# Kernel tuning notes

Measured on AMD Instinct MI355X. Metric: run time of the kernel, lower is better.

The kernel has to match this reference:

```python
import jax, jax.numpy as jnp
import numpy as np

B, S, D = 4, 2048, 1024
NEG_BIG = -1.0e9


def setup_inputs() -> dict:
    key = jax.random.key(0)
    ks = jax.random.split(key, 9)
    scale = 1.0 / np.sqrt(D)
    inp = {
        "v": jax.random.normal(ks[0], (B, S, D), dtype=jnp.float32),
        "k": jax.random.normal(ks[1], (B, S, D), dtype=jnp.float32),
        "q": jax.random.normal(ks[2], (B, S, D), dtype=jnp.float32),
        # causal mask: 1 where attention is disallowed (j > i), broadcast over batch
        "mask": jnp.triu(jnp.ones((1, S, S), dtype=jnp.float32), k=1),
        "Wq": jax.random.normal(ks[3], (D, D), dtype=jnp.float32) * scale,
        "bq": jnp.zeros((D,), dtype=jnp.float32),
        "Wk": jax.random.normal(ks[4], (D, D), dtype=jnp.float32) * scale,
        "bk": jnp.zeros((D,), dtype=jnp.float32),
        "Wv": jax.random.normal(ks[5], (D, D), dtype=jnp.float32) * scale,
        "bv": jnp.zeros((D,), dtype=jnp.float32),
    }
    return inp


def reference(v, k, q, mask, Wq, bq, Wk, bk, Wv, bv):
    # Dense projections (Keras Dense: x @ W + b)
    qp = q @ Wq + bq  # [B, S, D]
    kp = k @ Wk + bk  # [B, S, D]
    vp = v @ Wv + bv  # [B, S, D]

    dk = jnp.asarray(D, dtype=qp.dtype)
    logits = jnp.einsum("bqd,bkd->bqk", qp, kp) / jnp.sqrt(dk)  # [B, S, S]
    logits = logits + mask * NEG_BIG
    attn = jax.nn.softmax(logits, axis=-1)  # [B, S, S]
    out = jnp.einsum("bqk,bkd->bqd", attn, vp)  # [B, S, D]
    return out, attn
```

## Files before the change

### kernel.cpp

```cpp
#include <hip/hip_runtime.h>
#include <hip/hip_bf16.h>
#include <cstdint>

#define BATCH 4
#define S_LEN 2048
#define D_DIM 1024

typedef __attribute__((ext_vector_type(4))) float f32x4_t;
typedef __attribute__((ext_vector_type(8))) __bf16 bf16x8_t;

__device__ __forceinline__ ushort f32_to_bf16(float f) {
    uint32_t u = __float_as_uint(f);
    uint32_t r = (u + 0x7FFFu + ((u >> 16) & 1u)) >> 16;
    return (ushort)r;
}

__global__ __launch_bounds__(256)
void cvt_all_kernel(const float* __restrict__ q, const float* __restrict__ k,
                    const float* __restrict__ v, const float* __restrict__ wk,
                    const float* __restrict__ wq,
                    ushort* __restrict__ xqkv, ushort* __restrict__ xw, int n4) {
    int z = blockIdx.y;
    const float* src;
    ushort* dst;
    int n;
    if (z < 3) {
        src = (z == 0) ? q : ((z == 1) ? k : v);
        dst = xqkv + (size_t)z * n4 * 4;
        n = n4;
    } else {
        src = nullptr; dst = nullptr; n = 0;
    }
    int idx = blockIdx.x * blockDim.x + threadIdx.x;
    int stride = gridDim.x * blockDim.x;
    if (z < 3) {
        const float4* in4 = (const float4*)src;
        ushort4* out4 = (ushort4*)dst;
        for (int i = idx; i < n; i += stride) {
            float4 vv = in4[i];
            ushort4 o;
            o.x = f32_to_bf16(vv.x);
            o.y = f32_to_bf16(vv.y);
            o.z = f32_to_bf16(vv.z);
            o.w = f32_to_bf16(vv.w);
            out4[i] = o;
        }
    } else {
        int nw = D_DIM * D_DIM / 4;
        const float4* ik = (const float4*)wk;
        const float4* iq = (const float4*)wq;
        ushort4* ok = (ushort4*)xw;
        ushort4* oq = (ushort4*)(xw + (size_t)D_DIM * D_DIM);
        for (int i = idx; i < nw; i += stride) {
            float4 a = ik[i];
            ushort4 o;
            o.x = f32_to_bf16(a.x); o.y = f32_to_bf16(a.y);
            o.z = f32_to_bf16(a.z); o.w = f32_to_bf16(a.w);
            ok[i] = o;
            float4 b = iq[i];
            o.x = f32_to_bf16(b.x); o.y = f32_to_bf16(b.y);
            o.z = f32_to_bf16(b.z); o.w = f32_to_bf16(b.w);
            oq[i] = o;
        }
    }
}

__global__ __launch_bounds__(256)
void transpose_cvt_kernel(const float* __restrict__ in, ushort* __restrict__ out,
                          int rows, int cols) {
    __shared__ ushort tile[64][66];
    int r0 = blockIdx.y * 64, c0 = blockIdx.x * 64;
    int t = threadIdx.x;
    int cr = t & 63;
    int cc = t >> 6;
    #pragma unroll
    for (int i = 0; i < 16; ++i) {
        int r = cc * 16 + i;
        tile[r][cr] = f32_to_bf16(in[(size_t)(r0 + r) * cols + (c0 + cr)]);
    }
    __syncthreads();
    #pragma unroll
    for (int i = 0; i < 16; ++i) {
        int c = cc * 16 + i;
        out[(size_t)(c0 + c) * rows + (r0 + cr)] = tile[cr][c];
    }
}

__global__ __launch_bounds__(256)
void fill_kernel(const float* __restrict__ bv, float* __restrict__ bias2) {
    int i = blockIdx.x * blockDim.x + threadIdx.x;
    bias2[i] = (i < D_DIM) ? 0.f : bv[i - D_DIM];
}

__global__ __launch_bounds__(256)
void hv_kernel(const float* __restrict__ Wk, const float* __restrict__ bq,
               float* __restrict__ hv) {
    int wave = threadIdx.x >> 6, lane = threadIdx.x & 63;
    int r = blockIdx.x * 4 + wave;
    const float* row = Wk + (size_t)r * D_DIM;
    float s = 0.f;
    #pragma unroll
    for (int it = 0; it < 16; ++it)
        s += row[it * 64 + lane] * bq[it * 64 + lane];
    #pragma unroll
    for (int off = 32; off > 0; off >>= 1)
        s += __shfl_xor(s, off);
    if (lane == 0) hv[r] = s;
}

__global__ __launch_bounds__(256)
void wvec_kernel(const ushort* __restrict__ xk, const float* __restrict__ hv,
                 float* __restrict__ w) {
    int wave = threadIdx.x >> 6, lane = threadIdx.x & 63;
    int r = blockIdx.x * 4 + wave;
    const ushort* row = xk + (size_t)r * D_DIM + lane * 16;
    const float* hp = hv + lane * 16;
    float s = 0.f;
    #pragma unroll
    for (int it = 0; it < 16; ++it) {
        uint32_t u = row[it];
        s += __uint_as_float(u << 16) * hp[it];
    }
    #pragma unroll
    for (int off = 32; off > 0; off >>= 1)
        s += __shfl_xor(s, off);
    if (lane == 0) w[r] = s * 0.03125f;
}

enum { MODE_PROJ = 0, MODE_MT = 1, MODE_LOGITS = 2 };

#define PRE_BAR() do { __builtin_amdgcn_s_barrier(); \
    asm volatile("s_waitcnt lgkmcnt(0)" ::: "memory"); \
    __builtin_amdgcn_sched_barrier(0); } while (0)
#define POST_BAR() do { __builtin_amdgcn_sched_barrier(0); \
    __builtin_amdgcn_s_barrier(); } while (0)
#define GATE(N) do { asm volatile("s_waitcnt vmcnt(" #N ")" ::: "memory"); \
    __builtin_amdgcn_sched_barrier(0); } while (0)

#define GLOAD(dst, src) __builtin_amdgcn_global_load_lds( \
    (const __attribute__((address_space(1))) uint32_t*)(src), \
    (__attribute__((address_space(3))) uint32_t*)(dst), 16, 0, 0)

__device__ __forceinline__ void xcd_swizzle(int& bc, int& br) {
    int gx = gridDim.x;
    int nwg = gx * gridDim.y;
    int orig = blockIdx.y * gx + blockIdx.x;
    int xcd = orig & 7, idx = orig >> 3;
    int wgid = xcd * (nwg >> 3) + idx;
    bc = wgid % gx;
    br = wgid / gx;
}

template<int MODE>
__global__ __launch_bounds__(512, 2)
void gemm_q_kernel(const ushort* __restrict__ A, const ushort* __restrict__ Bt,
                   const float* __restrict__ bias, void* __restrict__ Cout,
                   ushort* __restrict__ vpTp,
                   int K, int lda, int ldb, int ldc,
                   long strideA, long strideC, float scale) {
    __shared__ ushort As[2][256 * 64];
    __shared__ ushort Bs[2][256 * 64];
    int bc, br;
    xcd_swizzle(bc, br);
    int bz = blockIdx.z;
    if (MODE == MODE_LOGITS && bc > br) return;
    const ushort* Ab = (MODE == MODE_PROJ) ? A + (size_t)(bc >> 2) * strideA
                                           : A + (size_t)bz * strideA;
    const ushort* Bb = (MODE == MODE_LOGITS) ? Bt + (size_t)bz * strideA : Bt;
    int brow = br * 256, bcol = bc * 256;
    int t = threadIdx.x, lane = t & 63, wid = t >> 6;
    int wr = wid >> 2, wc = wid & 3;
    int nkt = K / 64;

    const ushort* aSrc[4];
    const ushort* bSrc[4];
    int oL[4];
    #pragma unroll
    for (int j = 0; j < 4; ++j) {
        int o = (j * 512 + t) * 16;
        int row = o >> 7;
        int colb = (o & 127) ^ ((row & 7) << 4);
        oL[j] = o >> 1;
        aSrc[j] = Ab + (size_t)(brow + row) * lda + (colb >> 1);
        bSrc[j] = Bb + (size_t)(bcol + row) * ldb + (colb >> 1);
    }
    auto stgA = [&](int tk, int slot, int j0, int j1) {
        ushort* d = &As[slot][0];
        GLOAD(d + oL[j0], aSrc[j0] + tk * 64);
        GLOAD(d + oL[j1], aSrc[j1] + tk * 64);
    };
    auto stgB = [&](int tk, int slot, int j0, int j1) {
        ushort* d = &Bs[slot][0];
        GLOAD(d + oL[j0], bSrc[j0] + tk * 64);
        GLOAD(d + oL[j1], bSrc[j1] + tk * 64);
    };

    int rdA[2][4], rdB[4];
    #pragma unroll
    for (int mh = 0; mh < 2; ++mh)
        #pragma unroll
        for (int m = 0; m < 4; ++m) {
            int ra = wr * 128 + mh * 64 + m * 16 + (lane & 15);
            int cb = (lane >> 4) * 16;
            rdA[mh][m] = ra * 128 + (cb ^ ((ra & 7) << 4));
        }
    #pragma unroll
    for (int nf = 0; nf < 4; ++nf) {
        int rb = (nf >> 1) * 128 + wc * 32 + (nf & 1) * 16 + (lane & 15);
        int cb = (lane >> 4) * 16;
        rdB[nf] = rb * 128 + (cb ^ ((rb & 7) << 4));
    }

    f32x4_t acc[8][4];
    #pragma unroll
    for (int m = 0; m < 8; ++m)
        #pragma unroll
        for (int n = 0; n < 4; ++n)
            acc[m][n] = (f32x4_t){0.f, 0.f, 0.f, 0.f};

    bf16x8_t af[4][2], bfr[4][2];

    auto readAh = [&](int slot, int mh) {
        const char* base = (const char*)&As[slot][0];
        #pragma unroll
        for (int m = 0; m < 4; ++m) {
            af[m][0] = *(const bf16x8_t*)(base + rdA[mh][m]);
            af[m][1] = *(const bf16x8_t*)(base + (rdA[mh][m] ^ 64));
        }
    };
    auto readBh = [&](int slot, int nh) {
        const char* base = (const char*)&Bs[slot][0];
        #pragma unroll
        for (int n = 0; n < 2; ++n) {
            int nf = nh * 2 + n;
            bfr[nf][0] = *(const bf16x8_t*)(base + rdB[nf]);
            bfr[nf][1] = *(const bf16x8_t*)(base + (rdB[nf] ^ 64));
        }
    };

#define QUAD(MH, NH)                                                                \
    do { __builtin_amdgcn_s_setprio(1);                                             \
        _Pragma("unroll") for (int m = 0; m < 4; ++m)                               \
        _Pragma("unroll") for (int n = 0; n < 2; ++n)                               \
        _Pragma("unroll") for (int ks = 0; ks < 2; ++ks)                            \
            acc[(MH) * 4 + m][(NH) * 2 + n] = __builtin_amdgcn_mfma_f32_16x16x32_bf16( \
                af[m][ks], bfr[(NH) * 2 + n][ks], acc[(MH) * 4 + m][(NH) * 2 + n], 0, 0, 0); \
        __builtin_amdgcn_s_setprio(0); } while (0)

    stgB(0, 0, 0, 1); stgA(0, 0, 0, 2); stgB(0, 0, 2, 3); stgA(0, 0, 1, 3);
    GATE(4);
    __builtin_amdgcn_s_barrier();

    for (int y = 0; y < nkt; ++y) {
        int cur = y & 1, nxt = cur ^ 1;
        bool st = (y + 1 < nkt);
        readAh(cur, 0); readBh(cur, 0);
        if (st) stgB(y + 1, nxt, 0, 1);
        PRE_BAR(); QUAD(0, 0);
        if (st) { GATE(4); } else { GATE(2); }
        POST_BAR();
        readBh(cur, 1);
        if (st) stgA(y + 1, nxt, 0, 2);
        PRE_BAR(); QUAD(0, 1);
        if (st) { GATE(4); } else { GATE(0); }
        POST_BAR();
        readAh(cur, 1);
        if (st) stgB(y + 1, nxt, 2, 3);
        PRE_BAR(); QUAD(1, 1); POST_BAR();
        if (st) stgA(y + 1, nxt, 1, 3);
        PRE_BAR(); QUAD(1, 0);
        if (st) { GATE(4); }
        POST_BAR();
    }
#undef QUAD

    int crow0 = brow + wr * 128 + ((lane >> 4) * 4);
    int ccol0 = wc * 32 + (lane & 15);
    if (MODE == MODE_PROJ) {
        #pragma unroll
        for (int mf = 0; mf < 8; ++mf) {
            int rowg = crow0 + (mf >> 2) * 64 + (mf & 3) * 16;
            #pragma unroll
            for (int nf = 0; nf < 4; ++nf) {
                int gcol = bcol + (nf >> 1) * 128 + ccol0 + (nf & 1) * 16;
                float bv = bias[gcol];
                if (gcol < D_DIM) {
                    ushort* C = (ushort*)Cout;
                    #pragma unroll
                    for (int j = 0; j < 4; ++j)
                        C[(size_t)(rowg + j) * D_DIM + gcol] = f32_to_bf16(acc[mf][nf][j] + bv);
                } else {
                    int d = gcol - D_DIM;
                    int b = rowg >> 11, s = rowg & 2047;
                    ushort4 o;
                    o.x = f32_to_bf16(acc[mf][nf][0] + bv);
                    o.y = f32_to_bf16(acc[mf][nf][1] + bv);
                    o.z = f32_to_bf16(acc[mf][nf][2] + bv);
                    o.w = f32_to_bf16(acc[mf][nf][3] + bv);
                    *(ushort4*)&vpTp[((size_t)b * D_DIM + d) * S_LEN + s] = o;
                }
            }
        }
    } else if (MODE == MODE_MT) {
        ushort* C = (ushort*)Cout;
        #pragma unroll
        for (int mf = 0; mf < 8; ++mf) {
            int rowg = crow0 + (mf >> 2) * 64 + (mf & 3) * 16;
            #pragma unroll
            for (int nf = 0; nf < 4; ++nf) {
                int gcol = bcol + (nf >> 1) * 128 + ccol0 + (nf & 1) * 16;
                #pragma unroll
                for (int j = 0; j < 4; ++j)
                    C[(size_t)(rowg + j) * ldc + gcol] = f32_to_bf16(acc[mf][nf][j]);
            }
        }
    } else {
        float* C = (float*)Cout + (size_t)bz * strideC;
        #pragma unroll
        for (int mf = 0; mf < 8; ++mf) {
            int rowg = crow0 + (mf >> 2) * 64 + (mf & 3) * 16;
            #pragma unroll
            for (int nf = 0; nf < 4; ++nf) {
                int col = bcol + (nf >> 1) * 128 + ccol0 + (nf & 1) * 16;
                #pragma unroll
                for (int j = 0; j < 4; ++j)
                    C[(size_t)(rowg + j) * ldc + col] = acc[mf][nf][j] * scale;
            }
        }
    }
}

#define LGKM(N) do { asm volatile("s_waitcnt lgkmcnt(" #N ")" ::: "memory"); \
    __builtin_amdgcn_sched_barrier(0); } while (0)

__global__ __launch_bounds__(512, 2)
void gemm_out_kernel(const ushort* __restrict__ A, const ushort* __restrict__ Bt,
                     void* __restrict__ Cout,
                     int K, int lda, int ldb, int ldc,
                     long strideA, long strideB, long strideC, float scale) {
    __shared__ ushort As[3][256 * 64];
    __shared__ ushort Bs[3][128 * 64];
    int bc, br;
    xcd_swizzle(bc, br);
    int bz = blockIdx.z;
    const ushort* Ab = A + (size_t)bz * strideA;
    const ushort* Bb = Bt + (size_t)bz * strideB;
    int brow = br * 256, bcol = bc * 128;
    int t = threadIdx.x, lane = t & 63, wid = t >> 6;
    int wr = wid >> 1, wc = wid & 1;
    int nkt = min(K / 64, (brow + 256) / 64);

    const ushort* aSrc[4];
    const ushort* bSrc[2];
    int oA[4], oB[2];
    #pragma unroll
    for (int j = 0; j < 4; ++j) {
        int o = (j * 512 + t) * 16;
        int row = o >> 7;
        int col = (o & 127) ^ ((row & 7) << 4);
        oA[j] = o >> 1;
        aSrc[j] = Ab + (size_t)(brow + row) * lda + (col >> 1);
    }
    #pragma unroll
    for (int j = 0; j < 2; ++j) {
        int o = (j * 512 + t) * 16;
        int row = o >> 7;
        int col = (o & 127) ^ ((row & 7) << 4);
        oB[j] = o >> 1;
        bSrc[j] = Bb + (size_t)(bcol + row) * ldb + (col >> 1);
    }
    auto stage = [&](int tk, int slot) {
        ushort* dA = &As[slot][0];
        ushort* dB = &Bs[slot][0];
        #pragma unroll
        for (int j = 0; j < 4; ++j) GLOAD(dA + oA[j], aSrc[j] + tk * 64);
        #pragma unroll
        for (int j = 0; j < 2; ++j) GLOAD(dB + oB[j], bSrc[j] + tk * 64);
    };

    int rdA[4][2], rdB[4][2];
    #pragma unroll
    for (int m = 0; m < 4; ++m) {
        int ra = wr * 64 + m * 16 + (lane & 15);
        #pragma unroll
        for (int ks = 0; ks < 2; ++ks) {
            int cb = ks * 64 + ((lane >> 4) * 16);
            rdA[m][ks] = ra * 128 + (cb ^ ((ra & 7) << 4));
        }
    }
    #pragma unroll
    for (int n = 0; n < 4; ++n) {
        int rb = wc * 64 + n * 16 + (lane & 15);
        #pragma unroll
        for (int ks = 0; ks < 2; ++ks) {
            int cb = ks * 64 + ((lane >> 4) * 16);
            rdB[n][ks] = rb * 128 + (cb ^ ((rb & 7) << 4));
        }
    }

    f32x4_t acc[4][4];
    #pragma unroll
    for (int m = 0; m < 4; ++m)
        #pragma unroll
        for (int n = 0; n < 4; ++n)
            acc[m][n] = (f32x4_t){0.f, 0.f, 0.f, 0.f};

    bf16x8_t aE0[4], aE1[4], bE0[4], bE1[4];
    bf16x8_t aO0[4], aO1[4], bO0[4], bO1[4];

#define MF16(AV, BV)                                                           \
    do { __builtin_amdgcn_s_setprio(1);                                        \
        _Pragma("unroll") for (int m = 0; m < 4; ++m)                          \
        _Pragma("unroll") for (int n = 0; n < 4; ++n)                          \
            acc[m][n] = __builtin_amdgcn_mfma_f32_16x16x32_bf16(               \
                AV[m], BV[n], acc[m][n], 0, 0, 0);                             \
        __builtin_amdgcn_s_setprio(0); } while (0)

#define TILE_BODY(X, CA0, CA1, CB0, CB1, NA0, NA1, NB0, NB1)                   \
    do {                                                                       \
        int x_ = (X);                                                          \
        __builtin_amdgcn_s_barrier();                                          \
        if (x_ + 2 < nkt) stage(x_ + 2, (x_ + 2) % 3);                         \
        if (x_ + 1 < nkt) { if (x_ + 2 < nkt) { GATE(6); } else { GATE(0); } } \
        __builtin_amdgcn_s_barrier();                                          \
        {                                                                      \
            const char* nA = (const char*)&As[(x_ + 1) % 3][0];                \
            const char* nB = (const char*)&Bs[(x_ + 1) % 3][0];                \
            if (x_ + 1 < nkt) {                                                \
                _Pragma("unroll") for (int n = 0; n < 4; ++n)                  \
                    NB0[n] = *(const bf16x8_t*)(nB + rdB[n][0]);               \
                _Pragma("unroll") for (int m = 0; m < 4; ++m)                  \
                    NA0[m] = *(const bf16x8_t*)(nA + rdA[m][0]);               \
                LGKM(8);                                                       \
            } else { LGKM(0); }                                                \
            MF16(CA0, CB0);                                                    \
            if (x_ + 1 < nkt) {                                                \
                _Pragma("unroll") for (int n = 0; n < 4; ++n)                  \
                    NB1[n] = *(const bf16x8_t*)(nB + rdB[n][1]);               \
                _Pragma("unroll") for (int m = 0; m < 4; ++m)                  \
                    NA1[m] = *(const bf16x8_t*)(nA + rdA[m][1]);               \
            }                                                                  \
            MF16(CA1, CB1);                                                    \
        }                                                                      \
    } while (0)

    stage(0, 0);
    stage(1, 1);
    GATE(6);
    __builtin_amdgcn_s_barrier();
    {
        const char* pA = (const char*)&As[0][0];
        const char* pB = (const char*)&Bs[0][0];
        #pragma unroll
        for (int n = 0; n < 4; ++n) bE0[n] = *(const bf16x8_t*)(pB + rdB[n][0]);
        #pragma unroll
        for (int m = 0; m < 4; ++m) aE0[m] = *(const bf16x8_t*)(pA + rdA[m][0]);
        #pragma unroll
        for (int n = 0; n < 4; ++n) bE1[n] = *(const bf16x8_t*)(pB + rdB[n][1]);
        #pragma unroll
        for (int m = 0; m < 4; ++m) aE1[m] = *(const bf16x8_t*)(pA + rdA[m][1]);
    }

    int nhalf = nkt >> 1;
    for (int it = 0; it < nhalf; ++it) {
        int x = 2 * it;
        TILE_BODY(x,     aE0, aE1, bE0, bE1, aO0, aO1, bO0, bO1);
        TILE_BODY(x + 1, aO0, aO1, bO0, bO1, aE0, aE1, bE0, bE1);
    }
#undef TILE_BODY
#undef MF16

    float* C = (float*)Cout + (size_t)bz * strideC;
    int crow0 = brow + wr * 64 + ((lane >> 4) * 4);
    int ccol0 = bcol + wc * 64 + (lane & 15);
    #pragma unroll
    for (int mf = 0; mf < 4; ++mf)
        #pragma unroll
        for (int nf = 0; nf < 4; ++nf) {
            int col = ccol0 + nf * 16;
            #pragma unroll
            for (int j = 0; j < 4; ++j) {
                int rowg = crow0 + mf * 16 + j;
                C[(size_t)rowg * ldc + col] = acc[mf][nf][j] * scale;
            }
        }
}

__global__ __launch_bounds__(256)
void softmax_causal_kernel(float* __restrict__ attn, ushort* __restrict__ attn_bf,
                           const float* __restrict__ w) {
    int rowid = blockIdx.x;
    int i = rowid & (S_LEN - 1);
    float* lrow = attn + (size_t)rowid * S_LEN;
    ushort* brw = attn_bf + (size_t)rowid * S_LEN;
    const float* wv = w + (rowid & ~(S_LEN - 1));
    int t = threadIdx.x;
    int nvalid = i + 1;
    int nact = (nvalid + 255) >> 8;

    float vals[8];
    float lmax = -1e30f;
    #pragma unroll
    for (int it = 0; it < 8; ++it) {
        if (it < nact) {
            int j = it * 256 + t;
            float v = (j < nvalid) ? (lrow[j] + wv[j]) : -1e30f;
            vals[it] = v;
            lmax = fmaxf(lmax, v);
        }
    }
    #pragma unroll
    for (int off = 32; off > 0; off >>= 1)
        lmax = fmaxf(lmax, __shfl_xor(lmax, off));

    __shared__ float redm[4];
    __shared__ float reds[4];
    int wave = t >> 6, lane = t & 63;
    if (lane == 0) redm[wave] = lmax;
    __syncthreads();
    float m = fmaxf(fmaxf(redm[0], redm[1]), fmaxf(redm[2], redm[3]));

    float lsum = 0.f;
    #pragma unroll
    for (int it = 0; it < 8; ++it) {
        if (it < nact) {
            int j = it * 256 + t;
            float e = (j < nvalid) ? __expf(vals[it] - m) : 0.f;
            vals[it] = e;
            lsum += e;
        }
    }
    #pragma unroll
    for (int off = 32; off > 0; off >>= 1)
        lsum += __shfl_xor(lsum, off);
    if (lane == 0) reds[wave] = lsum;
    __syncthreads();
    float denom = reds[0] + reds[1] + reds[2] + reds[3];
    float inv = 1.f / denom;

    #pragma unroll
    for (int it = 0; it < 8; ++it) {
        int j = it * 256 + t;
        if (it < nact) {
            float p = vals[it] * inv;
            lrow[j] = p;
            brw[j] = f32_to_bf16(p);
        } else {
            lrow[j] = 0.f;
        }
    }
}

extern "C" void kernel_launch(void* const* d_in, const int* in_sizes, int n_in,
                              void* d_out, int out_size, void* d_ws, size_t ws_size,
                              hipStream_t stream) {
    const float* v  = (const float*)d_in[0];
    const float* k  = (const float*)d_in[1];
    const float* q  = (const float*)d_in[2];
    const float* Wq = (const float*)d_in[4];
    const float* bq = (const float*)d_in[5];
    const float* Wk = (const float*)d_in[6];
    const float* Wv = (const float*)d_in[8];
    const float* bv = (const float*)d_in[9];

    float* out  = (float*)d_out;
    float* attn = (float*)d_out + (size_t)BATCH * S_LEN * D_DIM;

    char* ws = (char*)d_ws;
    const size_t MB = 1024u * 1024u;
    const size_t NTOK = (size_t)BATCH * S_LEN;
    ushort* xqkv  = (ushort*)(ws);
    ushort* xq    = xqkv;
    ushort* xk    = xqkv + NTOK * D_DIM;
    ushort* qq    = (ushort*)(ws + 48 * MB);
    ushort* vpT   = (ushort*)(ws + 64 * MB);
    ushort* Bcat  = (ushort*)(ws + 80 * MB);
    ushort* xW    = (ushort*)(ws + 84 * MB);
    float*  bias2 = (float*)(ws + 88 * MB);
    float*  hvb   = (float*)(ws + 88 * MB + 8192);
    float*  wvec  = (float*)(ws + 88 * MB + 16384);
    ushort* attn_bf = (ushort*)(ws);

    const int n4 = (int)(NTOK * D_DIM / 4);
    cvt_all_kernel<<<dim3(1024, 4), dim3(256), 0, stream>>>(q, k, v, Wk, Wq, xqkv, xW, n4);
    transpose_cvt_kernel<<<dim3(16, 16), dim3(256), 0, stream>>>(Wv, Bcat + (size_t)D_DIM * D_DIM, D_DIM, D_DIM);
    fill_kernel<<<dim3(8), dim3(256), 0, stream>>>(bv, bias2);
    hv_kernel<<<dim3(256), dim3(256), 0, stream>>>(Wk, bq, hvb);
    wvec_kernel<<<dim3(2048), dim3(256), 0, stream>>>(xk, hvb, wvec);

    gemm_q_kernel<MODE_MT><<<dim3(4, 4, 1), dim3(512), 0, stream>>>(
        xW, xW + (size_t)D_DIM * D_DIM, nullptr, Bcat, nullptr,
        D_DIM, D_DIM, D_DIM, D_DIM, 0, 0, 1.f);

    gemm_q_kernel<MODE_PROJ><<<dim3(8, 32, 1), dim3(512), 0, stream>>>(
        xqkv, Bcat, bias2, qq, vpT,
        D_DIM, D_DIM, D_DIM, 2048, (long)2 * NTOK * D_DIM, 0, 1.f);

    gemm_q_kernel<MODE_LOGITS><<<dim3(8, 8, BATCH), dim3(512), 0, stream>>>(
        qq, xk, nullptr, attn, nullptr,
        D_DIM, D_DIM, D_DIM, S_LEN,
        (long)S_LEN * D_DIM, (long)S_LEN * S_LEN, 0.03125f);

    softmax_causal_kernel<<<dim3((int)NTOK), dim3(256), 0, stream>>>(attn, attn_bf, wvec);

    gemm_out_kernel<<<dim3(8, 8, BATCH), dim3(512), 0, stream>>>(
        attn_bf, vpT, out, S_LEN, S_LEN, S_LEN, D_DIM,
        (long)S_LEN * S_LEN, (long)D_DIM * S_LEN, (long)S_LEN * D_DIM, 1.f);
}
```

Before: 219.6 us.

## Split-K the weight-product and causal logits GEMMs to fill more CUs

```diff
diff --git a/kernel.cpp b/kernel.cpp
--- a/kernel.cpp
+++ b/kernel.cpp
@@ -1,5 +1,6 @@
 #include <hip/hip_runtime.h>
 #include <hip/hip_bf16.h>
+#include <hip/hip_fp16.h>
 #include <cstdint>
 
 #define BATCH 4
@@ -13,6 +14,14 @@
     uint32_t u = __float_as_uint(f);
     uint32_t r = (u + 0x7FFFu + ((u >> 16) & 1u)) >> 16;
     return (ushort)r;
+}
+__device__ __forceinline__ ushort f32_to_f16(float f) {
+    __half h = __float2half(f);
+    return *(ushort*)&h;
+}
+__device__ __forceinline__ float f16_to_f32(ushort u) {
+    __half h = *(__half*)&u;
+    return __half2float(h);
 }
 
 __global__ __launch_bounds__(256)
@@ -21,22 +30,14 @@
                     const float* __restrict__ wq,
                     ushort* __restrict__ xqkv, ushort* __restrict__ xw, int n4) {
     int z = blockIdx.y;
-    const float* src;
-    ushort* dst;
-    int n;
-    if (z < 3) {
-        src = (z == 0) ? q : ((z == 1) ? k : v);
-        dst = xqkv + (size_t)z * n4 * 4;
-        n = n4;
-    } else {
-        src = nullptr; dst = nullptr; n = 0;
-    }
     int idx = blockIdx.x * blockDim.x + threadIdx.x;
     int stride = gridDim.x * blockDim.x;
     if (z < 3) {
+        const float* src = (z == 0) ? q : ((z == 1) ? k : v);
+        ushort* dst = xqkv + (size_t)z * n4 * 4;
         const float4* in4 = (const float4*)src;
         ushort4* out4 = (ushort4*)dst;
-        for (int i = idx; i < n; i += stride) {
+        for (int i = idx; i < n4; i += stride) {
             float4 vv = in4[i];
             ushort4 o;
             o.x = f32_to_bf16(vv.x);
@@ -127,6 +128,22 @@
     if (lane == 0) w[r] = s * 0.03125f;
 }
 
+__global__ __launch_bounds__(256)
+void mt_reduce_kernel(const ushort* __restrict__ p, ushort* __restrict__ M) {
+    int i = blockIdx.x * 1024 + threadIdx.x * 4;
+    const size_t N = (size_t)D_DIM * D_DIM;
+    ushort4 a = *(const ushort4*)&p[i];
+    ushort4 b = *(const ushort4*)&p[N + i];
+    ushort4 c = *(const ushort4*)&p[2 * N + i];
+    ushort4 d = *(const ushort4*)&p[3 * N + i];
+    ushort4 o;
+    o.x = f32_to_bf16(f16_to_f32(a.x) + f16_to_f32(b.x) + f16_to_f32(c.x) + f16_to_f32(d.x));
+    o.y = f32_to_bf16(f16_to_f32(a.y) + f16_to_f32(b.y) + f16_to_f32(c.y) + f16_to_f32(d.y));
+    o.z = f32_to_bf16(f16_to_f32(a.z) + f16_to_f32(b.z) + f16_to_f32(c.z) + f16_to_f32(d.z));
+    o.w = f32_to_bf16(f16_to_f32(a.w) + f16_to_f32(b.w) + f16_to_f32(c.w) + f16_to_f32(d.w));
+    *(ushort4*)&M[i] = o;
+}
+
 enum { MODE_PROJ = 0, MODE_MT = 1, MODE_LOGITS = 2 };
 
 #define PRE_BAR() do { __builtin_amdgcn_s_barrier(); \
@@ -155,15 +172,37 @@
 __global__ __launch_bounds__(512, 2)
 void gemm_q_kernel(const ushort* __restrict__ A, const ushort* __restrict__ Bt,
                    const float* __restrict__ bias, void* __restrict__ Cout,
-                   ushort* __restrict__ vpTp,
+                   ushort* __restrict__ aux,
                    int K, int lda, int ldb, int ldc,
                    long strideA, long strideC, float scale) {
     __shared__ ushort As[2][256 * 64];
     __shared__ ushort Bs[2][256 * 64];
-    int bc, br;
-    xcd_swizzle(bc, br);
-    int bz = blockIdx.z;
-    if (MODE == MODE_LOGITS && bc > br) return;
+
+    int bc, br, bz = 0, kh = 0, tri = 0, koff = 0;
+    if (MODE == MODE_PROJ) {
+        xcd_swizzle(bc, br);
+    } else {
+        int nwg = gridDim.x;
+        int orig = blockIdx.x;
+        int widx = (orig & 7) * (nwg >> 3) + (orig >> 3);
+        if (MODE == MODE_MT) {
+            kh = widx & 3;
+            int tile = widx >> 2;
+            bc = tile & 3;
+            br = tile >> 2;
+            koff = kh << 8;
+        } else {
+            kh = widx & 1;
+            int rest = widx >> 1;
+            bz = rest / 36;
+            tri = rest - bz * 36;
+            br = 0;
+            while ((br + 1) * (br + 2) / 2 <= tri) ++br;
+            bc = tri - br * (br + 1) / 2;
+            koff = kh << 9;
+        }
+    }
+
     const ushort* Ab = (MODE == MODE_PROJ) ? A + (size_t)(bc >> 2) * strideA
                                            : A + (size_t)bz * strideA;
     const ushort* Bb = (MODE == MODE_LOGITS) ? Bt + (size_t)bz * strideA : Bt;
@@ -181,8 +220,8 @@
         int row = o >> 7;
         int colb = (o & 127) ^ ((row & 7) << 4);
         oL[j] = o >> 1;
-        aSrc[j] = Ab + (size_t)(brow + row) * lda + (colb >> 1);
-        bSrc[j] = Bb + (size_t)(bcol + row) * ldb + (colb >> 1);
+        aSrc[j] = Ab + (size_t)(brow + row) * lda + (colb >> 1) + koff;
+        bSrc[j] = Bb + (size_t)(bcol + row) * ldb + (colb >> 1) + koff;
     }
     auto stgA = [&](int tk, int slot, int j0, int j1) {
         ushort* d = &As[slot][0];
@@ -274,15 +313,15 @@
     }
 #undef QUAD
 
-    int crow0 = brow + wr * 128 + ((lane >> 4) * 4);
-    int ccol0 = wc * 32 + (lane & 15);
+    int lrow0 = wr * 128 + ((lane >> 4) * 4);
+    int lcol0 = wc * 32 + (lane & 15);
     if (MODE == MODE_PROJ) {
         #pragma unroll
         for (int mf = 0; mf < 8; ++mf) {
-            int rowg = crow0 + (mf >> 2) * 64 + (mf & 3) * 16;
+            int rowg = brow + lrow0 + (mf >> 2) * 64 + (mf & 3) * 16;
             #pragma unroll
             for (int nf = 0; nf < 4; ++nf) {
-                int gcol = bcol + (nf >> 1) * 128 + ccol0 + (nf & 1) * 16;
+                int gcol = bcol + (nf >> 1) * 128 + lcol0 + (nf & 1) * 16;
                 float bv = bias[gcol];
                 if (gcol < D_DIM) {
                     ushort* C = (ushort*)Cout;
@@ -297,34 +336,49 @@
                     o.y = f32_to_bf16(acc[mf][nf][1] + bv);
                     o.z = f32_to_bf16(acc[mf][nf][2] + bv);
                     o.w = f32_to_bf16(acc[mf][nf][3] + bv);
-                    *(ushort4*)&vpTp[((size_t)b * D_DIM + d) * S_LEN + s] = o;
+                    *(ushort4*)&aux[((size_t)b * D_DIM + d) * S_LEN + s] = o;
                 }
             }
         }
     } else if (MODE == MODE_MT) {
-        ushort* C = (ushort*)Cout;
+        ushort* P = aux + (size_t)kh * D_DIM * D_DIM;
         #pragma unroll
         for (int mf = 0; mf < 8; ++mf) {
-            int rowg = crow0 + (mf >> 2) * 64 + (mf & 3) * 16;
+            int rowg = brow + lrow0 + (mf >> 2) * 64 + (mf & 3) * 16;
             #pragma unroll
             for (int nf = 0; nf < 4; ++nf) {
-                int gcol = bcol + (nf >> 1) * 128 + ccol0 + (nf & 1) * 16;
+                int gcol = bcol + (nf >> 1) * 128 + lcol0 + (nf & 1) * 16;
                 #pragma unroll
                 for (int j = 0; j < 4; ++j)
-                    C[(size_t)(rowg + j) * ldc + gcol] = f32_to_bf16(acc[mf][nf][j]);
+                    P[(size_t)(rowg + j) * D_DIM + gcol] = f32_to_f16(acc[mf][nf][j]);
             }
         }
     } else {
-        float* C = (float*)Cout + (size_t)bz * strideC;
-        #pragma unroll
-        for (int mf = 0; mf < 8; ++mf) {
-            int rowg = crow0 + (mf >> 2) * 64 + (mf & 3) * 16;
+        if (kh == 0) {
+            float* C = (float*)Cout + (size_t)bz * strideC;
             #pragma unroll
-            for (int nf = 0; nf < 4; ++nf) {
-                int col = bcol + (nf >> 1) * 128 + ccol0 + (nf & 1) * 16;
+            for (int mf = 0; mf < 8; ++mf) {
+                int rowg = brow + lrow0 + (mf >> 2) * 64 + (mf & 3) * 16;
                 #pragma unroll
-                for (int j = 0; j < 4; ++j)
-                    C[(size_t)(rowg + j) * ldc + col] = acc[mf][nf][j] * scale;
+                for (int nf = 0; nf < 4; ++nf) {
+                    int col = bcol + (nf >> 1) * 128 + lcol0 + (nf & 1) * 16;
+                    #pragma unroll
+                    for (int j = 0; j < 4; ++j)
+                        C[(size_t)(rowg + j) * ldc + col] = acc[mf][nf][j] * scale;
+                }
+            }
+        } else {
+            ushort* P = aux + ((size_t)(bz * 36 + tri) << 16);
+            #pragma unroll
+            for (int mf = 0; mf < 8; ++mf) {
+                int lr = lrow0 + (mf >> 2) * 64 + (mf & 3) * 16;
+                #pragma unroll
+                for (int nf = 0; nf < 4; ++nf) {
+                    int lc = (nf >> 1) * 128 + lcol0 + (nf & 1) * 16;
+                    #pragma unroll
+                    for (int j = 0; j < 4; ++j)
+                        P[(size_t)(lr + j) * 256 + lc] = f32_to_f16(acc[mf][nf][j] * scale);
+                }
             }
         }
     }
@@ -488,15 +542,17 @@
 
 __global__ __launch_bounds__(256)
 void softmax_causal_kernel(float* __restrict__ attn, ushort* __restrict__ attn_bf,
-                           const float* __restrict__ w) {
+                           const float* __restrict__ w, const ushort* __restrict__ lgp) {
     int rowid = blockIdx.x;
+    int bz = rowid >> 11;
     int i = rowid & (S_LEN - 1);
+    int br = i >> 8;
     float* lrow = attn + (size_t)rowid * S_LEN;
     ushort* brw = attn_bf + (size_t)rowid * S_LEN;
     const float* wv = w + (rowid & ~(S_LEN - 1));
     int t = threadIdx.x;
     int nvalid = i + 1;
-    int nact = (nvalid + 255) >> 8;
+    int nact = br + 1;
 
     float vals[8];
     float lmax = -1e30f;
@@ -504,7 +560,9 @@
     for (int it = 0; it < 8; ++it) {
         if (it < nact) {
             int j = it * 256 + t;
-            float v = (j < nvalid) ? (lrow[j] + wv[j]) : -1e30f;
+            int tri = br * (br + 1) / 2 + it;
+            float lp = f16_to_f32(lgp[((size_t)(bz * 36 + tri) << 16) + ((i & 255) << 8) + t]);
+            float v = (j < nvalid) ? (lrow[j] + lp + wv[j]) : -1e30f;
             vals[it] = v;
             lmax = fmaxf(lmax, v);
         }
@@ -570,15 +628,16 @@
     const size_t MB = 1024u * 1024u;
     const size_t NTOK = (size_t)BATCH * S_LEN;
     ushort* xqkv  = (ushort*)(ws);
-    ushort* xq    = xqkv;
     ushort* xk    = xqkv + NTOK * D_DIM;
     ushort* qq    = (ushort*)(ws + 48 * MB);
     ushort* vpT   = (ushort*)(ws + 64 * MB);
     ushort* Bcat  = (ushort*)(ws + 80 * MB);
     ushort* xW    = (ushort*)(ws + 84 * MB);
-    float*  bias2 = (float*)(ws + 88 * MB);
-    float*  hvb   = (float*)(ws + 88 * MB + 8192);
-    float*  wvec  = (float*)(ws + 88 * MB + 16384);
+    ushort* mtp   = (ushort*)(ws + 88 * MB);
+    ushort* lgp   = (ushort*)(ws + 80 * MB);
+    float*  bias2 = (float*)(ws + 99 * MB);
+    float*  hvb   = (float*)(ws + 99 * MB + 8192);
+    float*  wvec  = (float*)(ws + 99 * MB + 16384);
     ushort* attn_bf = (ushort*)(ws);
 
     const int n4 = (int)(NTOK * D_DIM / 4);
@@ -588,20 +647,21 @@
     hv_kernel<<<dim3(256), dim3(256), 0, stream>>>(Wk, bq, hvb);
     wvec_kernel<<<dim3(2048), dim3(256), 0, stream>>>(xk, hvb, wvec);
 
-    gemm_q_kernel<MODE_MT><<<dim3(4, 4, 1), dim3(512), 0, stream>>>(
-        xW, xW + (size_t)D_DIM * D_DIM, nullptr, Bcat, nullptr,
-        D_DIM, D_DIM, D_DIM, D_DIM, 0, 0, 1.f);
+    gemm_q_kernel<MODE_MT><<<dim3(64), dim3(512), 0, stream>>>(
+        xW, xW + (size_t)D_DIM * D_DIM, nullptr, nullptr, mtp,
+        256, D_DIM, D_DIM, D_DIM, 0, 0, 1.f);
+    mt_reduce_kernel<<<dim3(1024), dim3(256), 0, stream>>>(mtp, Bcat);
 
     gemm_q_kernel<MODE_PROJ><<<dim3(8, 32, 1), dim3(512), 0, stream>>>(
         xqkv, Bcat, bias2, qq, vpT,
         D_DIM, D_DIM, D_DIM, 2048, (long)2 * NTOK * D_DIM, 0, 1.f);
 
-    gemm_q_kernel<MODE_LOGITS><<<dim3(8, 8, BATCH), dim3(512), 0, stream>>>(
-        qq, xk, nullptr, attn, nullptr,
-        D_DIM, D_DIM, D_DIM, S_LEN,
+    gemm_q_kernel<MODE_LOGITS><<<dim3(288), dim3(512), 0, stream>>>(
+        qq, xk, nullptr, attn, lgp,
+        512, D_DIM, D_DIM, S_LEN,
         (long)S_LEN * D_DIM, (long)S_LEN * S_LEN, 0.03125f);
 
-    softmax_causal_kernel<<<dim3((int)NTOK), dim3(256), 0, stream>>>(attn, attn_bf, wvec);
+    softmax_causal_kernel<<<dim3((int)NTOK), dim3(256), 0, stream>>>(attn, attn_bf, wvec, lgp);
 
     gemm_out_kernel<<<dim3(8, 8, BATCH), dim3(512), 0, stream>>>(
         attn_bf, vpT, out, S_LEN, S_LEN, S_LEN, D_DIM,
```

Measured after the change: 207.2 us. 5.6% less time.
